# Performance work log

Measured on AMD Instinct MI355X. Metric: run time of the kernel, lower is better.

## Reference

```python
import jax, jax.numpy as jnp
import numpy as np

EPS = 1e-10      # normalizer eps from the torch module
IN_EPS = 1e-5    # torch InstanceNorm2d default eps
STRIDE = 2
PAD = 1


def _dw_conv_transpose(x, W):
    """Depthwise ConvTranspose2d applied for every output channel at once.

    x: [B, Cin, H, W]
    W: [Cin, Cout, kh, kw]  (W[:, i] is sub_convs[i].weight of shape [Cin, 1, kh, kw])
    returns: [B, Cin, Cout, H', W'] where channel (c, i) = convT of x[:, c] with W[c, i].
    """
    Cin, Cout, kh, kw = W.shape
    # Transposed conv == dilated conv with spatially flipped kernel,
    # lhs_dilation = stride, padding = k - 1 - pad (output_padding = 0).
    rhs = jnp.flip(W, axis=(-2, -1)).reshape(Cin * Cout, 1, kh, kw)
    pad_h = (kh - 1 - PAD, kh - 1 - PAD)
    pad_w = (kw - 1 - PAD, kw - 1 - PAD)
    out = jax.lax.conv_general_dilated(
        x, rhs,
        window_strides=(1, 1),
        padding=(pad_h, pad_w),
        lhs_dilation=(STRIDE, STRIDE),
        dimension_numbers=('NCHW', 'OIHW', 'NCHW'),
        feature_group_count=Cin,
    )  # [B, Cin*Cout, H', W'], group-major: group c -> channels c*Cout:(c+1)*Cout
    B = x.shape[0]
    return out.reshape(B, Cin, Cout, out.shape[2], out.shape[3])


def setup_inputs() -> dict:
    key = jax.random.key(0)
    k1, k2, k3 = jax.random.split(key, 3)
    B, Cin, Cout, H, Wd, K = 2, 64, 64, 48, 48, 4
    x = jax.random.normal(k1, (B, Cin, H, Wd), dtype=jnp.float32)
    # Positive-leaning weights keep the normalizer (convT of ones) away from zero.
    W = 0.05 + 0.1 * jax.random.uniform(k2, (Cin, Cout, K, K), dtype=jnp.float32)
    bias = 0.02 * jax.random.normal(k3, (Cout,), dtype=jnp.float32)
    return {"x": x, "W": W, "bias": bias}


def reference(x, W, bias):
    # numerator: depthwise convT of the input for every (in_ch, out_ch) pair
    num = _dw_conv_transpose(x, W)                       # [B, Cin, Cout, H', W']
    # normalizer: same convT applied to ones (batch-independent -> batch of 1)
    den = _dw_conv_transpose(jnp.ones_like(x[:1]), W) + EPS  # [1, Cin, Cout, H', W']
    out = jnp.sum(num / den, axis=1) + bias[None, :, None, None]  # [B, Cout, H', W']
    # InstanceNorm2d (no affine, biased variance) over spatial dims per (b, c)
    mean = jnp.mean(out, axis=(2, 3), keepdims=True)
    var = jnp.var(out, axis=(2, 3), keepdims=True)
    return (out - mean) / jnp.sqrt(var + IN_EPS)
```

## Files before the change

### kernel.cpp

```cpp
#include <hip/hip_runtime.h>
#include <hip/hip_fp16.h>

#define BB    2
#define CIN   64
#define NI    64
#define HIN   48
#define WIN   48
#define HO    96
#define WO    96
#define EPSN  1e-10f
#define IN_EPS 1e-5f
#define IMG   (HO*WO)
#define NIMG  (BB*NI)
#define CS    8
#define NC    (CIN/CS)

#define TW    52
#define TROWS 50
#define TILE  (TROWS*TW)

__device__ __align__(16) __half2 g_part[CS * NIMG * (IMG / 2)];

__global__ __launch_bounds__(192, 2) void conv_kernel(
        const float* __restrict__ x, const float* __restrict__ Wt) {
    const int bi = blockIdx.x, s = blockIdx.y;
    const int b = bi >> 6, i = bi & 63, c0 = s * NC;
    const int tid = threadIdx.x;
    const int ty = tid / 12, tx = tid - 12 * ty;

    __shared__ __align__(16) float sX[2][TILE];
    __shared__ __align__(16) float sF[NC * 16];
    __shared__ float sW[NC * 16];
    __shared__ float sR[NC * 16];
    __shared__ float sFix[384];

    {
        const float4 z = make_float4(0.f, 0.f, 0.f, 0.f);
        for (int e = tid; e < 2 * TROWS; e += 192) {
            const int q = e / TROWS, row = e - q * TROWS;
            float* rp = &sX[q][row * TW];
            if (row == 0 || row == TROWS - 1) {
#pragma unroll
                for (int k = 0; k < TW; k += 4) *(float4*)(rp + k) = z;
            } else {
                *(float4*)(rp + 48) = z;
            }
        }
    }

    for (int e = tid; e < NC * 16; e += 192) {
        const int c = e >> 4, j = e & 15;
        const float* wp = Wt + ((size_t)(c0 + c) * NI + i) * 16;
        sW[e] = wp[j];
        const int py = (j >> 3) & 1, px = (j >> 2) & 1, a = (j >> 1) & 1, bb = j & 1;
        const int kh = py ? (a ? 2 : 0) : (a ? 3 : 1);
        const int kw = px ? (bb ? 2 : 0) : (bb ? 3 : 1);
        const int r0 = py ? 0 : 1, r1 = py ? 2 : 3;
        const int q0 = px ? 0 : 1, q1 = px ? 2 : 3;
        const float den = wp[r0 * 4 + q0] + wp[r0 * 4 + q1]
                        + wp[r1 * 4 + q0] + wp[r1 * 4 + q1];
        sF[e] = wp[kh * 4 + kw] / (den + EPSN);
        const int cy = j >> 2, cx = j & 3;
        const int THn[4] = {1, 2, 2, 1};
        const int THv[4][2] = {{1, 1}, {0, 2}, {1, 3}, {2, 2}};
        float den2 = 0.f;
        for (int aa = 0; aa < THn[cy]; ++aa)
            for (int bb2 = 0; bb2 < THn[cx]; ++bb2)
                den2 += wp[THv[cy][aa] * 4 + THv[cx][bb2]];
        sR[e] = 1.f / (den2 + EPSN);
    }

    int ldsOff[3];
#pragma unroll
    for (int k = 0; k < 3; ++k) {
        const int e = tid + 192 * k;
        const int row = e / 12, c4 = e - 12 * row;
        ldsOff[k] = (row + 1) * TW + 4 * c4;
    }
    const float4* xg = (const float4*)x + (size_t)(b * CIN + c0) * 576;

    const int rowBase = 3 * ty;
    const int cMain = 4 * tx;
    const int cE0 = (tx == 0) ? 48 : 4 * tx - 1;
    const int cE5 = (tx == 11) ? 48 : 4 * tx + 4;

    int qA0[2], qA1[2], qB0[2], qB1[2], wI[2][4], clsI[2];
#pragma unroll
    for (int k = 0; k < 2; ++k) {
        const int p = tid + 192 * k;
        if (k == 1 && p >= 380) break;
        int y, xo;
        if (p < 96)       { y = 0;            xo = p; }
        else if (p < 192) { y = 95;           xo = p - 96; }
        else if (p < 286) { y = p - 192 + 1;  xo = 0; }
        else              { y = p - 286 + 1;  xo = 95; }
        const int hA = (y + 1) >> 1, hB = hA - 1;
        const int khA = (y & 1) ? 0 : 1, khB = khA + 2;
        const int wA = (xo + 1) >> 1, wB = wA - 1;
        const int kwA = (xo & 1) ? 0 : 1, kwB = kwA + 2;
        const int colA = wA;
        const int colB = (wB < 0) ? 48 : wB;
        const int rA = (hA + 1) * TW, rB = (hB + 1) * TW;
        qA0[k] = rA + colA; qA1[k] = rA + colB;
        qB0[k] = rB + colA; qB1[k] = rB + colB;
        wI[k][0] = khA * 4 + kwA; wI[k][1] = khA * 4 + kwB;
        wI[k][2] = khB * 4 + kwA; wI[k][3] = khB * 4 + kwB;
        const int cy = (y == 0) ? 0 : (y == 95) ? 3 : ((y & 1) ? 1 : 2);
        const int cx = (xo == 0) ? 0 : (xo == 95) ? 3 : ((xo & 1) ? 1 : 2);
        clsI[k] = cy * 4 + cx;
    }

    __syncthreads();

    {
        const float4 a0 = xg[tid], a1 = xg[tid + 192], a2 = xg[tid + 384];
        float* d = &sX[0][0];
        *(float4*)(d + ldsOff[0]) = a0;
        *(float4*)(d + ldsOff[1]) = a1;
        *(float4*)(d + ldsOff[2]) = a2;
    }
    __syncthreads();

    float acc[6][8];
#pragma unroll
    for (int r = 0; r < 6; ++r)
#pragma unroll
        for (int j = 0; j < 8; ++j) acc[r][j] = 0.f;
    float fixAcc0 = 0.f, fixAcc1 = 0.f;

#pragma unroll 2
    for (int c = 0; c < NC; ++c) {
        float4 a0, a1, a2;
        if (c + 1 < NC) {
            const float4* xn = xg + (size_t)(c + 1) * 576;
            a0 = xn[tid]; a1 = xn[tid + 192]; a2 = xn[tid + 384];
        }

        float g[16];
        {
            const float4* gf = (const float4*)&sF[c * 16];
#pragma unroll
            for (int q = 0; q < 4; ++q) {
                const float4 t = gf[q];
                g[4 * q] = t.x; g[4 * q + 1] = t.y;
                g[4 * q + 2] = t.z; g[4 * q + 3] = t.w;
            }
        }

        const float* __restrict__ xs = &sX[c & 1][0];

        float xv[5][6];
#pragma unroll
        for (int pr = 0; pr < 5; ++pr) {
            const int ro = (rowBase + pr) * TW;
            xv[pr][0] = xs[ro + cE0];
            const float4 m = *(const float4*)(xs + ro + cMain);
            xv[pr][1] = m.x; xv[pr][2] = m.y; xv[pr][3] = m.z; xv[pr][4] = m.w;
            xv[pr][5] = xs[ro + cE5];
        }

#pragma unroll
        for (int r = 0; r < 6; ++r) {
            const int prA = ((r + 1) >> 1) + 1, prB = prA - 1;
            const int py = r & 1;
#pragma unroll
            for (int j = 0; j < 8; ++j) {
                const int pcA = ((j + 1) >> 1) + 1, pcB = pcA - 1;
                const int px = j & 1;
                const float* gg = &g[py * 8 + px * 4];
                acc[r][j] += xv[prA][pcA] * gg[0] + xv[prA][pcB] * gg[1]
                           + xv[prB][pcA] * gg[2] + xv[prB][pcB] * gg[3];
            }
        }

        {
            const float* wc = &sW[c * 16];
            const float num0 = xs[qA0[0]] * wc[wI[0][0]] + xs[qA1[0]] * wc[wI[0][1]]
                             + xs[qB0[0]] * wc[wI[0][2]] + xs[qB1[0]] * wc[wI[0][3]];
            fixAcc0 += num0 * sR[c * 16 + clsI[0]];
            if (tid < 188) {
                const float num1 = xs[qA0[1]] * wc[wI[1][0]] + xs[qA1[1]] * wc[wI[1][1]]
                                 + xs[qB0[1]] * wc[wI[1][2]] + xs[qB1[1]] * wc[wI[1][3]];
                fixAcc1 += num1 * sR[c * 16 + clsI[1]];
            }
        }

        if (c + 1 < NC) {
            float* d = &sX[(c + 1) & 1][0];
            *(float4*)(d + ldsOff[0]) = a0;
            *(float4*)(d + ldsOff[1]) = a1;
            *(float4*)(d + ldsOff[2]) = a2;
        }
        __syncthreads();
    }

    sFix[tid] = fixAcc0;
    if (tid < 188) sFix[192 + tid] = fixAcc1;
    __syncthreads();

#pragma unroll
    for (int r = 0; r < 6; ++r)
#pragma unroll
        for (int j = 0; j < 8; ++j) {
            const int y = 6 * ty + r, xo = 8 * tx + j;
            if (y == 0)        acc[r][j] = sFix[xo];
            else if (y == 95)  acc[r][j] = sFix[96 + xo];
            else if (xo == 0)  acc[r][j] = sFix[192 + y - 1];
            else if (xo == 95) acc[r][j] = sFix[286 + y - 1];
        }

    {
        __half2* pp = g_part + ((size_t)s * NIMG + bi) * (IMG / 2)
                    + (6 * ty) * (WO / 2) + 4 * tx;
#pragma unroll
        for (int r = 0; r < 6; ++r) {
            __half2 h[4];
#pragma unroll
            for (int q = 0; q < 4; ++q)
                h[q] = __floats2half2_rn(acc[r][2 * q], acc[r][2 * q + 1]);
            *(float4*)(pp + r * (WO / 2)) = *(float4*)h;
        }
    }
}

__global__ __launch_bounds__(768) void epilogue_kernel(
        const float* __restrict__ bias, float* __restrict__ out) {
    const int bi = blockIdx.x;
    const int tid = threadIdx.x;
    const float bv = bias[bi & 63];
    const __half2* pb = g_part + (size_t)bi * (IMG / 2);
    const size_t stride2 = (size_t)NIMG * (IMG / 2);

    float4 v[3];
    float s1 = 0.f, s2 = 0.f;
#pragma unroll
    for (int k = 0; k < 3; ++k) {
        const int idx2 = (k * 768 + tid) * 2;
        float ax = 0.f, ay = 0.f, az = 0.f, aw = 0.f;
#pragma unroll
        for (int sp = 0; sp < CS; ++sp) {
            const float2 raw = *(const float2*)(pb + sp * stride2 + idx2);
            const __half2 h0 = ((const __half2*)&raw)[0];
            const __half2 h1 = ((const __half2*)&raw)[1];
            const float2 f0 = __half22float2(h0);
            const float2 f1 = __half22float2(h1);
            ax += f0.x; ay += f0.y; az += f1.x; aw += f1.y;
        }
        float4 t;
        t.x = ax + bv; t.y = ay + bv; t.z = az + bv; t.w = aw + bv;
        v[k] = t;
        s1 += t.x + t.y + t.z + t.w;
        s2 += t.x * t.x + t.y * t.y + t.z * t.z + t.w * t.w;
    }

    __shared__ float red[24];
    __shared__ float stat[2];
#pragma unroll
    for (int off = 32; off > 0; off >>= 1) {
        s1 += __shfl_down(s1, off, 64);
        s2 += __shfl_down(s2, off, 64);
    }
    const int w = tid >> 6;
    if ((tid & 63) == 0) { red[w] = s1; red[12 + w] = s2; }
    __syncthreads();
    if (tid == 0) {
        float t1 = 0.f, t2 = 0.f;
#pragma unroll
        for (int k = 0; k < 12; ++k) { t1 += red[k]; t2 += red[12 + k]; }
        const float mean = t1 * (1.f / 9216.f);
        const float m2 = t2 * (1.f / 9216.f);
        stat[0] = mean;
        stat[1] = rsqrtf(m2 - mean * mean + IN_EPS);
    }
    __syncthreads();
    const float mean = stat[0], inv = stat[1];

    float4* ob = (float4*)out + (size_t)bi * (IMG / 4);
#pragma unroll
    for (int k = 0; k < 3; ++k) {
        const int idx = k * 768 + tid;
        float4 t = v[k];
        t.x = (t.x - mean) * inv; t.y = (t.y - mean) * inv;
        t.z = (t.z - mean) * inv; t.w = (t.w - mean) * inv;
        ob[idx] = t;
    }
}

extern "C" void kernel_launch(void* const* d_in, const int* in_sizes, int n_in,
                              void* d_out, int out_size, void* d_ws, size_t ws_size,
                              hipStream_t stream) {
    const float* x    = (const float*)d_in[0];
    const float* Wt   = (const float*)d_in[1];
    const float* bias = (const float*)d_in[2];
    float* out = (float*)d_out;
    (void)d_ws; (void)ws_size;

    conv_kernel<<<dim3(NIMG, CS), 192, 0, stream>>>(x, Wt);
    epilogue_kernel<<<NIMG, 768, 0, stream>>>(bias, out);
}
```

Before: 91.42 us.

## Halve channel split, process two channels per barrier, prefold border weights

Result: no change. 93.20 us (+1.9%).

```diff
diff --git a/kernel.cpp b/kernel.cpp
--- a/kernel.cpp
+++ b/kernel.cpp
@@ -12,8 +12,9 @@
 #define IN_EPS 1e-5f
 #define IMG   (HO*WO)
 #define NIMG  (BB*NI)
-#define CS    8
+#define CS    4
 #define NC    (CIN/CS)
+#define GRP   (NC/2)
 
 #define TW    52
 #define TROWS 50
@@ -28,17 +29,16 @@
     const int tid = threadIdx.x;
     const int ty = tid / 12, tx = tid - 12 * ty;
 
-    __shared__ __align__(16) float sX[2][TILE];
+    __shared__ __align__(16) float sXf[4 * TILE];
     __shared__ __align__(16) float sF[NC * 16];
-    __shared__ float sW[NC * 16];
-    __shared__ float sR[NC * 16];
+    __shared__ __align__(16) float sB[NC * 64];
     __shared__ float sFix[384];
 
     {
         const float4 z = make_float4(0.f, 0.f, 0.f, 0.f);
-        for (int e = tid; e < 2 * TROWS; e += 192) {
+        for (int e = tid; e < 4 * TROWS; e += 192) {
             const int q = e / TROWS, row = e - q * TROWS;
-            float* rp = &sX[q][row * TW];
+            float* rp = &sXf[q * TILE + row * TW];
             if (row == 0 || row == TROWS - 1) {
 #pragma unroll
                 for (int k = 0; k < TW; k += 4) *(float4*)(rp + k) = z;
@@ -51,7 +51,6 @@
     for (int e = tid; e < NC * 16; e += 192) {
         const int c = e >> 4, j = e & 15;
         const float* wp = Wt + ((size_t)(c0 + c) * NI + i) * 16;
-        sW[e] = wp[j];
         const int py = (j >> 3) & 1, px = (j >> 2) & 1, a = (j >> 1) & 1, bb = j & 1;
         const int kh = py ? (a ? 2 : 0) : (a ? 3 : 1);
         const int kw = px ? (bb ? 2 : 0) : (bb ? 3 : 1);
@@ -60,22 +59,32 @@
         const float den = wp[r0 * 4 + q0] + wp[r0 * 4 + q1]
                         + wp[r1 * 4 + q0] + wp[r1 * 4 + q1];
         sF[e] = wp[kh * 4 + kw] / (den + EPSN);
-        const int cy = j >> 2, cx = j & 3;
+    }
+    for (int e = tid; e < NC * 64; e += 192) {
+        const int c = e >> 6, r = e & 63;
+        const int cls = r >> 2, t = r & 3;
+        const int cy = cls >> 2, cx = cls & 3;
+        const float* wp = Wt + ((size_t)(c0 + c) * NI + i) * 16;
         const int THn[4] = {1, 2, 2, 1};
         const int THv[4][2] = {{1, 1}, {0, 2}, {1, 3}, {2, 2}};
         float den2 = 0.f;
         for (int aa = 0; aa < THn[cy]; ++aa)
             for (int bb2 = 0; bb2 < THn[cx]; ++bb2)
                 den2 += wp[THv[cy][aa] * 4 + THv[cx][bb2]];
-        sR[e] = 1.f / (den2 + EPSN);
-    }
-
-    int ldsOff[3];
+        const float Rv = 1.f / (den2 + EPSN);
+        const int khA = (cy & 1) ? 0 : 1;
+        const int kwA = (cx & 1) ? 0 : 1;
+        const int kh = (t >> 1) ? khA + 2 : khA;
+        const int kw = (t & 1) ? kwA + 2 : kwA;
+        sB[e] = wp[kh * 4 + kw] * Rv;
+    }
+
+    int offA[3];
 #pragma unroll
     for (int k = 0; k < 3; ++k) {
         const int e = tid + 192 * k;
         const int row = e / 12, c4 = e - 12 * row;
-        ldsOff[k] = (row + 1) * TW + 4 * c4;
+        offA[k] = (row + 1) * TW + 4 * c4;
     }
     const float4* xg = (const float4*)x + (size_t)(b * CIN + c0) * 576;
 
@@ -84,7 +93,7 @@
     const int cE0 = (tx == 0) ? 48 : 4 * tx - 1;
     const int cE5 = (tx == 11) ? 48 : 4 * tx + 4;
 
-    int qA0[2], qA1[2], qB0[2], qB1[2], wI[2][4], clsI[2];
+    int qA0[2], qA1[2], qB0[2], qB1[2], clsI[2];
 #pragma unroll
     for (int k = 0; k < 2; ++k) {
         const int p = tid + 192 * k;
@@ -95,16 +104,12 @@
         else if (p < 286) { y = p - 192 + 1;  xo = 0; }
         else              { y = p - 286 + 1;  xo = 95; }
         const int hA = (y + 1) >> 1, hB = hA - 1;
-        const int khA = (y & 1) ? 0 : 1, khB = khA + 2;
         const int wA = (xo + 1) >> 1, wB = wA - 1;
-        const int kwA = (xo & 1) ? 0 : 1, kwB = kwA + 2;
         const int colA = wA;
         const int colB = (wB < 0) ? 48 : wB;
         const int rA = (hA + 1) * TW, rB = (hB + 1) * TW;
         qA0[k] = rA + colA; qA1[k] = rA + colB;
         qB0[k] = rB + colA; qB1[k] = rB + colB;
-        wI[k][0] = khA * 4 + kwA; wI[k][1] = khA * 4 + kwB;
-        wI[k][2] = khB * 4 + kwA; wI[k][3] = khB * 4 + kwB;
         const int cy = (y == 0) ? 0 : (y == 95) ? 3 : ((y & 1) ? 1 : 2);
         const int cx = (xo == 0) ? 0 : (xo == 95) ? 3 : ((xo & 1) ? 1 : 2);
         clsI[k] = cy * 4 + cx;
@@ -113,11 +118,12 @@
     __syncthreads();
 
     {
-        const float4 a0 = xg[tid], a1 = xg[tid + 192], a2 = xg[tid + 384];
-        float* d = &sX[0][0];
-        *(float4*)(d + ldsOff[0]) = a0;
-        *(float4*)(d + ldsOff[1]) = a1;
-        *(float4*)(d + ldsOff[2]) = a2;
+        float* d = &sXf[0];
+#pragma unroll
+        for (int k = 0; k < 3; ++k) {
+            *(float4*)(d + offA[k]) = xg[tid + 192 * k];
+            *(float4*)(d + TILE + offA[k]) = xg[576 + tid + 192 * k];
+        }
     }
     __syncthreads();
 
@@ -128,68 +134,78 @@
         for (int j = 0; j < 8; ++j) acc[r][j] = 0.f;
     float fixAcc0 = 0.f, fixAcc1 = 0.f;
 
-#pragma unroll 2
-    for (int c = 0; c < NC; ++c) {
-        float4 a0, a1, a2;
-        if (c + 1 < NC) {
-            const float4* xn = xg + (size_t)(c + 1) * 576;
-            a0 = xn[tid]; a1 = xn[tid + 192]; a2 = xn[tid + 384];
-        }
-
-        float g[16];
-        {
-            const float4* gf = (const float4*)&sF[c * 16];
-#pragma unroll
-            for (int q = 0; q < 4; ++q) {
-                const float4 t = gf[q];
-                g[4 * q] = t.x; g[4 * q + 1] = t.y;
-                g[4 * q + 2] = t.z; g[4 * q + 3] = t.w;
-            }
-        }
-
-        const float* __restrict__ xs = &sX[c & 1][0];
-
-        float xv[5][6];
-#pragma unroll
-        for (int pr = 0; pr < 5; ++pr) {
-            const int ro = (rowBase + pr) * TW;
-            xv[pr][0] = xs[ro + cE0];
-            const float4 m = *(const float4*)(xs + ro + cMain);
-            xv[pr][1] = m.x; xv[pr][2] = m.y; xv[pr][3] = m.z; xv[pr][4] = m.w;
-            xv[pr][5] = xs[ro + cE5];
-        }
-
-#pragma unroll
-        for (int r = 0; r < 6; ++r) {
-            const int prA = ((r + 1) >> 1) + 1, prB = prA - 1;
-            const int py = r & 1;
-#pragma unroll
-            for (int j = 0; j < 8; ++j) {
-                const int pcA = ((j + 1) >> 1) + 1, pcB = pcA - 1;
-                const int px = j & 1;
-                const float* gg = &g[py * 8 + px * 4];
-                acc[r][j] += xv[prA][pcA] * gg[0] + xv[prA][pcB] * gg[1]
-                           + xv[prB][pcA] * gg[2] + xv[prB][pcB] * gg[3];
-            }
-        }
-
-        {
-            const float* wc = &sW[c * 16];
-            const float num0 = xs[qA0[0]] * wc[wI[0][0]] + xs[qA1[0]] * wc[wI[0][1]]
-                             + xs[qB0[0]] * wc[wI[0][2]] + xs[qB1[0]] * wc[wI[0][3]];
-            fixAcc0 += num0 * sR[c * 16 + clsI[0]];
-            if (tid < 188) {
-                const float num1 = xs[qA0[1]] * wc[wI[1][0]] + xs[qA1[1]] * wc[wI[1][1]]
-                                 + xs[qB0[1]] * wc[wI[1][2]] + xs[qB1[1]] * wc[wI[1][3]];
-                fixAcc1 += num1 * sR[c * 16 + clsI[1]];
-            }
-        }
-
-        if (c + 1 < NC) {
-            float* d = &sX[(c + 1) & 1][0];
-            *(float4*)(d + ldsOff[0]) = a0;
-            *(float4*)(d + ldsOff[1]) = a1;
-            *(float4*)(d + ldsOff[2]) = a2;
+    for (int g = 0; g < GRP; ++g) {
+        float4 a[6];
+        if (g + 1 < GRP) {
+            const float4* xn = xg + (size_t)(2 * g + 2) * 576;
+#pragma unroll
+            for (int k = 0; k < 3; ++k) {
+                a[k]     = xn[tid + 192 * k];
+                a[k + 3] = xn[576 + tid + 192 * k];
+            }
+        }
+
+        const float* bufBase = &sXf[(g & 1) * 2 * TILE];
+
+#pragma unroll
+        for (int cg = 0; cg < 2; ++cg) {
+            const int c = 2 * g + cg;
+            const float* __restrict__ xs = bufBase + cg * TILE;
+
+            float gw[16];
+            {
+                const float4* gf = (const float4*)&sF[c * 16];
+#pragma unroll
+                for (int q = 0; q < 4; ++q) {
+                    const float4 t = gf[q];
+                    gw[4 * q] = t.x; gw[4 * q + 1] = t.y;
+                    gw[4 * q + 2] = t.z; gw[4 * q + 3] = t.w;
+                }
+            }
+
+            float xv[5][6];
+#pragma unroll
+            for (int pr = 0; pr < 5; ++pr) {
+                const int ro = (rowBase + pr) * TW;
+                xv[pr][0] = xs[ro + cE0];
+                const float4 m = *(const float4*)(xs + ro + cMain);
+                xv[pr][1] = m.x; xv[pr][2] = m.y; xv[pr][3] = m.z; xv[pr][4] = m.w;
+                xv[pr][5] = xs[ro + cE5];
+            }
+
+#pragma unroll
+            for (int r = 0; r < 6; ++r) {
+                const int prA = ((r + 1) >> 1) + 1, prB = prA - 1;
+                const int py = r & 1;
+#pragma unroll
+                for (int j = 0; j < 8; ++j) {
+                    const int pcA = ((j + 1) >> 1) + 1, pcB = pcA - 1;
+                    const int px = j & 1;
+                    const float* gg = &gw[py * 8 + px * 4];
+                    acc[r][j] += xv[prA][pcA] * gg[0] + xv[prA][pcB] * gg[1]
+                               + xv[prB][pcA] * gg[2] + xv[prB][pcB] * gg[3];
+                }
+            }
+
+            {
+                const float4 wb0 = *(const float4*)&sB[c * 64 + clsI[0] * 4];
+                fixAcc0 += xs[qA0[0]] * wb0.x + xs[qA1[0]] * wb0.y
+                         + xs[qB0[0]] * wb0.z + xs[qB1[0]] * wb0.w;
+                if (tid < 188) {
+                    const float4 wb1 = *(const float4*)&sB[c * 64 + clsI[1] * 4];
+                    fixAcc1 += xs[qA0[1]] * wb1.x + xs[qA1[1]] * wb1.y
+                             + xs[qB0[1]] * wb1.z + xs[qB1[1]] * wb1.w;
+                }
+            }
+        }
+
+        if (g + 1 < GRP) {
+            float* d = &sXf[((g + 1) & 1) * 2 * TILE];
+#pragma unroll
+            for (int k = 0; k < 3; ++k) {
+                *(float4*)(d + offA[k]) = a[k];
+                *(float4*)(d + TILE + offA[k]) = a[k + 3];
+            }
         }
         __syncthreads();
     }
```
